# Kernel optimization log

Measured on AMD Instinct MI355X. Metric: run time of the kernel, lower is better.

Reference implementation:

```python
import jax, jax.numpy as jnp
import numpy as np

B, IC, OC, K, H, W = 8, 512, 512, 3, 32, 32
GAIN, LRMUL = 1.0, 1.0
# compute_runtime_coef: fan_in = prod(weight_shape[:-1])
RC_CONV = GAIN / np.sqrt(K * K * IC) * LRMUL   # conv weight [K,K,IC,OC]
RC_DENSE = GAIN / np.sqrt(IC) * LRMUL          # dense weight [IC, IC]


def setup_inputs() -> dict:
    key = jax.random.key(0)
    ks = jax.random.split(key, 4)
    x = jax.random.normal(ks[0], (B, IC, H, W), dtype=jnp.float32)
    w = jax.random.normal(ks[1], (B, IC), dtype=jnp.float32)
    # init_std = 1/lrmul = 1.0 for both weights; bias init zeros
    conv_w = jax.random.normal(ks[2], (K, K, IC, OC), dtype=jnp.float32)
    dense_w = jax.random.normal(ks[3], (IC, IC), dtype=jnp.float32)
    dense_b = jnp.zeros((IC,), dtype=jnp.float32)
    return {"x": x, "w": w, "conv_w": conv_w, "dense_w": dense_w, "dense_b": dense_b}


def reference(x, w, conv_w, dense_w, dense_b):
    b, ic, h, wd = x.shape
    # modulation: style = Dense(w) + bias + 1
    style = w @ (RC_DENSE * dense_w) + LRMUL * dense_b + 1.0        # [B, IC]
    wt = (RC_CONV * conv_w)[None] * style[:, None, None, :, None]   # [B,K,K,IC,OC]
    # demodulation: rsqrt of sum of squares over (kh, kw, ic)
    d = jax.lax.rsqrt(jnp.sum(jnp.square(wt), axis=(1, 2, 3)) + 1e-8)  # [B, OC]
    wt = wt * d[:, None, None, None, :]
    # grouped conv with groups = batch: weight -> OIHW [B*OC, IC, K, K]
    w_g = jnp.transpose(wt, (0, 4, 3, 1, 2)).reshape(b * OC, ic, K, K)
    xg = x.reshape(1, b * ic, h, wd)
    y = jax.lax.conv_general_dilated(
        xg, w_g, window_strides=(1, 1), padding="SAME",
        dimension_numbers=("NCHW", "OIHW", "NCHW"), feature_group_count=b)
    return y.reshape(b, OC, h, wd)
```

## Files before the change

### kernel.cpp

```cpp
#include <hip/hip_runtime.h>
#include <stdint.h>


#define B_   8
#define IC_  512
#define OC_  512

static constexpr float RC_DENSE = 0.04419417382415922f;
static constexpr float RC_CONV  = 0.014731391274719739f;

typedef _Float16 half8    __attribute__((ext_vector_type(8)));
typedef float    floatx16 __attribute__((ext_vector_type(16)));

__device__ __forceinline__ void g2l(const void* g, void* l) {
  __builtin_amdgcn_global_load_lds(
      (const __attribute__((address_space(1))) void*)g,
      (__attribute__((address_space(3))) void*)l, 16, 0, 0);
}

__global__ __launch_bounds__(256) void style_kernel(
    const float* __restrict__ wv, const float* __restrict__ dw,
    const float* __restrict__ db, float* __restrict__ sm,
    float* __restrict__ sm2) {
  const int b = blockIdx.y;
  const int i = blockIdx.x * 64 + (threadIdx.x & 63);
  const int jg = threadIdx.x >> 6;
  __shared__ float red[4][64];
  float p = 0.f;
  for (int j = jg * 128; j < jg * 128 + 128; ++j)
    p += wv[b * IC_ + j] * dw[(size_t)j * IC_ + i];
  red[jg][threadIdx.x & 63] = p;
  __syncthreads();
  if (threadIdx.x < 64) {
    float s = red[0][threadIdx.x] + red[1][threadIdx.x] +
              red[2][threadIdx.x] + red[3][threadIdx.x];
    s = s * RC_DENSE + db[i] + 1.0f;
    float v = s * RC_CONV;
    sm[b * IC_ + i] = v;
    sm2[b * IC_ + i] = v * v;
  }
}

__global__ __launch_bounds__(256) void prep_kernel(
    const float* __restrict__ cw, const float* __restrict__ x,
    const float* __restrict__ sm, const float* __restrict__ sm2,
    _Float16* __restrict__ Wtf, float* __restrict__ dpart,
    _Float16* __restrict__ xsp) {
  __shared__ __align__(16) char smem[33280];
  const int bid = blockIdx.x;
  const int tid = threadIdx.x;
  if (bid < 256) {
    _Float16* LA = (_Float16*)smem;
    float* redall = (float*)(smem + 18432);
    const int by2 = bid >> 4, icb = bid & 15;
    const int by = by2 >> 1, h2 = by2 & 1;
    const int oc0 = by * 64 + h2 * 32, ic0 = icb * 32;
    const int ocl = tid & 31, g = tid >> 5;
    float sq4[4] = {};
    for (int m = 0; m < 36; ++m) {
      int r = m * 8 + g;
      int t = r >> 5, icl = r & 31;
      float v = cw[(size_t)(t * IC_ + ic0 + icl) * OC_ + oc0 + ocl];
      sq4[m & 3] += v * v;
      LA[m * 256 + ocl * 8 + g] = (_Float16)v;
    }
    for (int b = 0; b < 8; ++b) {
      float p = 0.f;
      for (int s = 0; s < 4; ++s)
        p += sm2[b * IC_ + ic0 + g + 8 * s] * sq4[s];
      redall[(b * 8 + g) * 32 + ocl] = p;
    }
    __syncthreads();
    _Float16* dst = Wtf + (size_t)(by * 16 + icb) * 18432;
    for (int it = 0; it < 5; ++it) {
      int c = it * 256 + tid;
      if (c < 1152) {
        int m = c >> 5, o2 = c & 31;
        *(half8*)(dst + (size_t)(m * 64 + h2 * 32 + o2) * 8) =
            *(const half8*)&LA[m * 256 + o2 * 8];
      }
    }
    const int bb = tid >> 5, o3 = tid & 31;
    float s = 0.f;
    for (int g2 = 0; g2 < 8; ++g2) s += redall[(bb * 8 + g2) * 32 + o3];
    dpart[(size_t)icb * 4096 + bb * OC_ + oc0 + o3] = s;
  } else {
    _Float16* Xt = (_Float16*)smem;
    const int rb = bid - 256;
    const int b = rb >> 5, h = rb & 31;
    for (int k = 0; k < 16; ++k) {
      int idx = k * 256 + tid;
      int ic = idx >> 3, wc = (idx & 7) * 4;
      float4 v = *(const float4*)&x[((size_t)(b * IC_ + ic) * 32 + h) * 32 + wc];
      float s = sm[b * IC_ + ic];
      Xt[(wc + 0) * 520 + ic] = (_Float16)(v.x * s);
      Xt[(wc + 1) * 520 + ic] = (_Float16)(v.y * s);
      Xt[(wc + 2) * 520 + ic] = (_Float16)(v.z * s);
      Xt[(wc + 3) * 520 + ic] = (_Float16)(v.w * s);
    }
    __syncthreads();
    _Float16* xb = xsp + (size_t)b * 16 * 36992;
    const int r = h + 1;
    half8 z = {};
    for (int it = 0; it < 9; ++it) {
      int c = it * 256 + tid;
      if (c < 2176) {
        int icb = c / 136, rem = c - 136 * icb, kkq = rem / 34, C = rem - 34 * kkq;
        half8 val = z;
        if (C != 0 && C != 33)
          val = *(const half8*)&Xt[(C - 1) * 520 + icb * 32 + kkq * 8];
        *(half8*)&xb[(size_t)icb * 36992 + (size_t)r * 1088 + kkq * 272 + C * 8] = val;
      }
    }
    if (h == 0 || h == 31) {
      const int rz = (h == 0) ? 0 : 33;
      for (int it = 0; it < 9; ++it) {
        int c = it * 256 + tid;
        if (c < 2176) {
          int icb = c / 136, rem = c - 136 * icb, kkq = rem / 34, C = rem - 34 * kkq;
          *(half8*)&xb[(size_t)icb * 36992 + (size_t)rz * 1088 + kkq * 272 + C * 8] = z;
        }
      }
    }
  }
}

__global__ __launch_bounds__(256, 4) void conv_kernel(
    const _Float16* __restrict__ Wtf,
    const _Float16* __restrict__ xsp,
    const float* __restrict__ dpart,
    float* __restrict__ out) {
  const int byq = blockIdx.x & 7, hoc = blockIdx.x >> 3;
  const int bx = blockIdx.y, b = blockIdx.z;
  const int tid = threadIdx.x, lane = tid & 63, w = tid >> 6;
  const int n = lane & 31, kq = lane >> 5;
  const int h0 = bx * 4;

  __shared__ __align__(16) _Float16 As[2][4608];
  __shared__ __align__(16) _Float16 Xs[2][3264];
  __shared__ float redd[8][32];
  __shared__ float dvl[32];

  const _Float16* gX = xsp + (size_t)b * 16 * 36992 + (size_t)h0 * 1088;
  const _Float16* gA = Wtf + (size_t)byq * 16 * 18432 + hoc * 256;

  auto stage = [&](int st, int p) {
    const int icb = st >> 1, kk = st & 1;
    const _Float16* a = gA + (size_t)icb * 18432 + kk * 1024;
    const _Float16* xg = gX + (size_t)icb * 36992 + kk * 544;
    if (w < 2) {
#pragma unroll
      for (int k = 0; k < 4; ++k) {
        int c = (w * 4 + k) * 64 + lane;
        int r = c >> 5, o2 = c & 31;
        g2l(a + ((r >> 1) * 4 + (r & 1)) * 512 + o2 * 8, &As[p][c * 8]);
      }
    } else if (w == 2) {
      {
        int c = 8 * 64 + lane;
        int r = c >> 5, o2 = c & 31;
        g2l(a + ((r >> 1) * 4 + (r & 1)) * 512 + o2 * 8, &As[p][c * 8]);
      }
#pragma unroll
      for (int k = 0; k < 3; ++k) {
        int c = k * 64 + lane;
        int r = c / 68, o = c - r * 68;
        g2l(xg + r * 1088 + o * 8, &Xs[p][c * 8]);
      }
    } else {
#pragma unroll
      for (int k = 0; k < 3; ++k) {
        int c = (3 + k) * 64 + lane;
        int r = c / 68, o = c - r * 68;
        g2l(xg + r * 1088 + o * 8, &Xs[p][c * 8]);
      }
      {
        int c = 6 * 64 + lane;
        if (lane < 24) {
          int r = c / 68, o = c - r * 68;
          g2l(xg + r * 1088 + o * 8, &Xs[p][c * 8]);
        }
      }
    }
  };

  floatx16 acc = {};
  stage(0, 0);
  for (int st = 0; st < 32; ++st) {
    const int cur = st & 1;
    if (st + 1 < 32) {
      stage(st + 1, cur ^ 1);
      asm volatile("s_waitcnt vmcnt(4)" ::: "memory");
    } else {
      asm volatile("s_waitcnt vmcnt(0)" ::: "memory");
    }
    __builtin_amdgcn_s_barrier();
    __builtin_amdgcn_sched_barrier(0);
    const _Float16* Ap = &As[cur][0] + kq * 256 + n * 8;
    const _Float16* Xp = &Xs[cur][0] + w * 544 + kq * 272 + n * 8;
    half8 a[9];
#pragma unroll
    for (int t = 0; t < 9; ++t) a[t] = *(const half8*)(Ap + t * 512);
#pragma unroll
    for (int s = 0; s < 3; ++s) {
#pragma unroll
      for (int kw = 0; kw < 3; ++kw) {
        half8 xv = *(const half8*)(Xp + s * 544 + kw * 8);
        acc = __builtin_amdgcn_mfma_f32_32x32x16_f16(a[s * 3 + kw], xv, acc,
                                                     0, 0, 0);
      }
    }
    __builtin_amdgcn_sched_barrier(0);
    __builtin_amdgcn_s_barrier();
  }

  const int oc0 = byq * 64 + hoc * 32;
  __syncthreads();
  {
    const int oc_l = tid & 31, ig = tid >> 5;
    float s = dpart[(size_t)(ig * 2) * 4096 + b * OC_ + oc0 + oc_l] +
              dpart[(size_t)(ig * 2 + 1) * 4096 + b * OC_ + oc0 + oc_l];
    redd[ig][oc_l] = s;
  }
  __syncthreads();
  if (tid < 32) {
    float s = 1e-8f;
#pragma unroll
    for (int g = 0; g < 8; ++g) s += redd[g][tid];
    dvl[tid] = rsqrtf(s);
  }
  __syncthreads();
#pragma unroll
  for (int rg = 0; rg < 16; ++rg) {
    const int row = (rg & 3) + 8 * (rg >> 2) + 4 * kq;
    float* op = out + ((size_t)b * OC_ + oc0 + row) * 1024 + (h0 + w) * 32 + n;
    op[0] = acc[rg] * dvl[row];
  }
}

extern "C" void kernel_launch(void* const* d_in, const int* in_sizes, int n_in,
                              void* d_out, int out_size, void* d_ws, size_t ws_size,
                              hipStream_t stream) {
  const float* x       = (const float*)d_in[0];
  const float* w       = (const float*)d_in[1];
  const float* conv_w  = (const float*)d_in[2];
  const float* dense_w = (const float*)d_in[3];
  const float* dense_b = (const float*)d_in[4];
  float* out = (float*)d_out;

  char* ws = (char*)d_ws;
  float*    sm    = (float*)ws;
  float*    sm2   = (float*)(ws + (16 << 10));
  float*    dpart = (float*)(ws + (32 << 10));
  _Float16* Wtf   = (_Float16*)(ws + (288 << 10));
  _Float16* xsp   = (_Float16*)(ws + (288 << 10) + 4718592);

  style_kernel<<<dim3(8, B_), 256, 0, stream>>>(w, dense_w, dense_b, sm, sm2);
  prep_kernel<<<512, 256, 0, stream>>>(conv_w, x, sm, sm2, Wtf, dpart, xsp);
  conv_kernel<<<dim3(16, 8, B_), 256, 0, stream>>>(Wtf, xsp, dpart, out);
}
```

Baseline: 132.9 us.

## Compute two output rows per wave to reuse input rows across kh taps

Each conv block now covers 8 output rows instead of 4. Each wave accumulates two rows, reusing every loaded input row fragment across up to two kernel-row taps, so fewer input rows are staged per output row. The staging split across waves is rebalanced for the larger X tile. MFMA sections get raised scheduling priority. This halves the grid to 512 blocks and lowers launch bounds occupancy to 2, which raises register and LDS use and may reduce latency hiding.

Result: faster. 127.9 us (-3.7%).

```diff
diff --git a/kernel.cpp b/kernel.cpp
--- a/kernel.cpp
+++ b/kernel.cpp
@@ -125,7 +125,7 @@
   }
 }
 
-__global__ __launch_bounds__(256, 4) void conv_kernel(
+__global__ __launch_bounds__(256, 2) void conv_kernel(
     const _Float16* __restrict__ Wtf,
     const _Float16* __restrict__ xsp,
     const float* __restrict__ dpart,
@@ -134,10 +134,10 @@
   const int bx = blockIdx.y, b = blockIdx.z;
   const int tid = threadIdx.x, lane = tid & 63, w = tid >> 6;
   const int n = lane & 31, kq = lane >> 5;
-  const int h0 = bx * 4;
+  const int h0 = bx * 8;
 
   __shared__ __align__(16) _Float16 As[2][4608];
-  __shared__ __align__(16) _Float16 Xs[2][3264];
+  __shared__ __align__(16) _Float16 Xs[2][5440];
   __shared__ float redd[8][32];
   __shared__ float dvl[32];
 
@@ -148,35 +148,41 @@
     const int icb = st >> 1, kk = st & 1;
     const _Float16* a = gA + (size_t)icb * 18432 + kk * 1024;
     const _Float16* xg = gX + (size_t)icb * 36992 + kk * 544;
-    if (w < 2) {
-#pragma unroll
-      for (int k = 0; k < 4; ++k) {
-        int c = (w * 4 + k) * 64 + lane;
+    if (w == 0) {
+#pragma unroll
+      for (int k = 0; k < 5; ++k) {
+        int c = k * 64 + lane;
         int r = c >> 5, o2 = c & 31;
         g2l(a + ((r >> 1) * 4 + (r & 1)) * 512 + o2 * 8, &As[p][c * 8]);
       }
-    } else if (w == 2) {
-      {
-        int c = 8 * 64 + lane;
+    } else if (w == 1) {
+#pragma unroll
+      for (int k = 0; k < 4; ++k) {
+        int c = (5 + k) * 64 + lane;
         int r = c >> 5, o2 = c & 31;
         g2l(a + ((r >> 1) * 4 + (r & 1)) * 512 + o2 * 8, &As[p][c * 8]);
       }
-#pragma unroll
-      for (int k = 0; k < 3; ++k) {
-        int c = k * 64 + lane;
+      {
+        int c = lane, r = c / 68, o = c - r * 68;
+        g2l(xg + r * 1088 + o * 8, &Xs[p][c * 8]);
+      }
+    } else if (w == 2) {
+#pragma unroll
+      for (int k = 0; k < 5; ++k) {
+        int c = (1 + k) * 64 + lane;
         int r = c / 68, o = c - r * 68;
         g2l(xg + r * 1088 + o * 8, &Xs[p][c * 8]);
       }
     } else {
 #pragma unroll
-      for (int k = 0; k < 3; ++k) {
-        int c = (3 + k) * 64 + lane;
+      for (int k = 0; k < 4; ++k) {
+        int c = (6 + k) * 64 + lane;
         int r = c / 68, o = c - r * 68;
         g2l(xg + r * 1088 + o * 8, &Xs[p][c * 8]);
       }
       {
-        int c = 6 * 64 + lane;
-        if (lane < 24) {
+        int c = 640 + lane;
+        if (lane < 40) {
           int r = c / 68, o = c - r * 68;
           g2l(xg + r * 1088 + o * 8, &Xs[p][c * 8]);
         }
@@ -184,32 +190,39 @@
     }
   };
 
-  floatx16 acc = {};
+  floatx16 acc[2] = {};
   stage(0, 0);
   for (int st = 0; st < 32; ++st) {
     const int cur = st & 1;
     if (st + 1 < 32) {
       stage(st + 1, cur ^ 1);
-      asm volatile("s_waitcnt vmcnt(4)" ::: "memory");
+      asm volatile("s_waitcnt vmcnt(5)" ::: "memory");
     } else {
       asm volatile("s_waitcnt vmcnt(0)" ::: "memory");
     }
     __builtin_amdgcn_s_barrier();
     __builtin_amdgcn_sched_barrier(0);
     const _Float16* Ap = &As[cur][0] + kq * 256 + n * 8;
-    const _Float16* Xp = &Xs[cur][0] + w * 544 + kq * 272 + n * 8;
+    const _Float16* Xp = &Xs[cur][0] + (2 * w) * 544 + kq * 272 + n * 8;
     half8 a[9];
 #pragma unroll
     for (int t = 0; t < 9; ++t) a[t] = *(const half8*)(Ap + t * 512);
-#pragma unroll
-    for (int s = 0; s < 3; ++s) {
+    __builtin_amdgcn_s_setprio(1);
+#pragma unroll
+    for (int s = 0; s < 4; ++s) {
 #pragma unroll
       for (int kw = 0; kw < 3; ++kw) {
         half8 xv = *(const half8*)(Xp + s * 544 + kw * 8);
-        acc = __builtin_amdgcn_mfma_f32_32x32x16_f16(a[s * 3 + kw], xv, acc,
-                                                     0, 0, 0);
-      }
-    }
+#pragma unroll
+        for (int kh = 0; kh < 3; ++kh) {
+          int j = s - kh;
+          if (j >= 0 && j < 2)
+            acc[j] = __builtin_amdgcn_mfma_f32_32x32x16_f16(
+                a[kh * 3 + kw], xv, acc[j], 0, 0, 0);
+        }
+      }
+    }
+    __builtin_amdgcn_s_setprio(0);
     __builtin_amdgcn_sched_barrier(0);
     __builtin_amdgcn_s_barrier();
   }
@@ -230,11 +243,14 @@
     dvl[tid] = rsqrtf(s);
   }
   __syncthreads();
+  const int r0 = h0 + 2 * w;
 #pragma unroll
   for (int rg = 0; rg < 16; ++rg) {
     const int row = (rg & 3) + 8 * (rg >> 2) + 4 * kq;
-    float* op = out + ((size_t)b * OC_ + oc0 + row) * 1024 + (h0 + w) * 32 + n;
-    op[0] = acc[rg] * dvl[row];
+    const float dv = dvl[row];
+    float* op = out + ((size_t)b * OC_ + oc0 + row) * 1024 + r0 * 32 + n;
+    op[0]  = acc[0][rg] * dv;
+    op[32] = acc[1][rg] * dv;
   }
 }
 
@@ -257,5 +273,5 @@
 
   style_kernel<<<dim3(8, B_), 256, 0, stream>>>(w, dense_w, dense_b, sm, sm2);
   prep_kernel<<<512, 256, 0, stream>>>(conv_w, x, sm, sm2, Wtf, dpart, xsp);
-  conv_kernel<<<dim3(16, 8, B_), 256, 0, stream>>>(Wtf, xsp, dpart, out);
-}
+  conv_kernel<<<dim3(16, 4, B_), 256, 0, stream>>>(Wtf, xsp, dpart, out);
+}
```
